# Kernel optimization log

Hardware: AMD Instinct MI355X
Metric: run time of the kernel (lower is better)

## Reference

```python
import jax, jax.numpy as jnp
import numpy as np


def setup_inputs() -> dict:
    key = jax.random.key(0)
    k1, k2 = jax.random.split(key)
    B, C, N, M = 8, 3, 4096, 4096
    source_point_cloud = jax.random.normal(k1, (B, C, N), dtype=jnp.float32)
    target_point_cloud = jax.random.normal(k2, (B, C, M), dtype=jnp.float32)
    return {"source_point_cloud": source_point_cloud,
            "target_point_cloud": target_point_cloud}


def _nn_indices(source, target):
    # source: [B,3,N], target: [B,3,M]
    # squared Euclidean distance: |s|^2 + |t|^2 - 2 s.t  (monotone in true distance,
    # so argmin matches the KD-tree nearest-neighbor query)
    s2 = jnp.sum(source * source, axis=1)               # [B,N]
    t2 = jnp.sum(target * target, axis=1)               # [B,M]
    cross = jnp.einsum('bcn,bcm->bnm', source, target)  # [B,N,M]
    d2 = s2[:, :, None] + t2[:, None, :] - 2.0 * cross  # [B,N,M]
    return jnp.argmin(d2, axis=2)                       # [B,N]


def reference(source_point_cloud, target_point_cloud):
    # Per-batch: nearest target point for each source point, then mean MSE.
    idx = _nn_indices(source_point_cloud, target_point_cloud)        # [B,N]
    # gather matched target points: [B,3,N]
    matched = jnp.take_along_axis(target_point_cloud, idx[:, None, :], axis=2)
    diff = source_point_cloud - matched
    # MSELoss over the (1,3,N) batch slice -> mean over 3*N elements; one scalar per batch
    loss_per_batch = jnp.mean(diff * diff, axis=(1, 2))              # [B]
    return loss_per_batch
```

## Files before the change

kernel.cpp:

```cpp
#include <hip/hip_runtime.h>


#define B_ 8
#define N_ 4096
#define CH 4096
#define BS 12288
#define TQ 512
#define BIG 3.4e38f

__global__ __launch_bounds__(512, 8)
void nn_loss_main(const float* __restrict__ src,
                  const float* __restrict__ tgt,
                  float* __restrict__ partial) {
    __shared__ __align__(16) char smem[8 * TQ * 4];
    float4* stage = (float4*)smem;
    float*  red   = (float*)smem;

    const int tid  = threadIdx.x;
    const int blk  = blockIdx.x;
    const int b    = blk >> 6;
    const int e    = (blk >> 3) & 7;
    const int sgrp = blk & 7;
    const int ls   = tid & 63;
    const int w    = tid >> 6;

    {
        const float* tb = tgt + b * BS;
        const int m = (e << 9) + tid;
        float x = tb[m], y = tb[m + CH], z = tb[m + 2 * CH];
        stage[tid] = make_float4(x, y, z, x * x + y * y + z * z);
    }

    const float* sb = src + b * BS;
    float ax[8], ay[8], az[8];
    #pragma unroll
    for (int j = 0; j < 8; ++j) {
        int n = (sgrp << 9) + (j << 6) + ls;
        ax[j] = -2.0f * sb[n];
        ay[j] = -2.0f * sb[n + CH];
        az[j] = -2.0f * sb[n + 2 * CH];
    }

    __syncthreads();

    float best[8];
    #pragma unroll
    for (int j = 0; j < 8; ++j) best[j] = BIG;

    const float4* tp = stage + (w << 6);
    #pragma unroll 2
    for (int i = 0; i < 64; i += 2) {
        float4 t0 = tp[i];
        float4 t1 = tp[i + 1];
        #pragma unroll
        for (int j = 0; j < 8; ++j) {
            float d0 = fmaf(ax[j], t0.x, fmaf(ay[j], t0.y, fmaf(az[j], t0.z, t0.w)));
            float d1 = fmaf(ax[j], t1.x, fmaf(ay[j], t1.y, fmaf(az[j], t1.z, t1.w)));
            best[j] = fminf(fminf(best[j], d0), d1);
        }
    }

    __syncthreads();

    #pragma unroll
    for (int j = 0; j < 8; ++j) {
        float s2 = 0.25f * fmaf(ax[j], ax[j], fmaf(ay[j], ay[j], az[j] * az[j]));
        red[(w << 9) + (j << 6) + ls] = best[j] + s2;
    }

    __syncthreads();

    float mn = red[tid];
    #pragma unroll
    for (int v = 1; v < 8; ++v)
        mn = fminf(mn, red[(v << 9) + tid]);
    partial[(e << 15) + (b << 12) + (sgrp << 9) + tid] = mn;
}

__global__ __launch_bounds__(1024)
void reduce_kernel(const float* __restrict__ partial,
                   float* __restrict__ out) {
    const int b = blockIdx.x;
    const int tid = threadIdx.x;

    float acc = 0.0f;
    #pragma unroll
    for (int j = 0; j < 4; ++j) {
        int base = (b << 12) + (j << 10) + tid;
        float mn = partial[base];
        #pragma unroll
        for (int e = 1; e < 8; ++e)
            mn = fminf(mn, partial[(e << 15) + base]);
        acc += mn;
    }

    #pragma unroll
    for (int off = 32; off > 0; off >>= 1)
        acc += __shfl_down(acc, off, 64);

    __shared__ float red[16];
    if ((tid & 63) == 0) red[tid >> 6] = acc;
    __syncthreads();
    if (tid == 0) {
        float v = 0.0f;
        #pragma unroll
        for (int k = 0; k < 16; ++k) v += red[k];
        out[b] = v * (1.0f / (3.0f * (float)N_));
    }
}

extern "C" void kernel_launch(void* const* d_in, const int* in_sizes, int n_in,
                              void* d_out, int out_size, void* d_ws, size_t ws_size,
                              hipStream_t stream) {
    const float* src = (const float*)d_in[0];
    const float* tgt = (const float*)d_in[1];
    float* out = (float*)d_out;
    float* partial = (float*)d_ws;

    nn_loss_main<<<512, 512, 0, stream>>>(src, tgt, partial);
    reduce_kernel<<<B_, 1024, 0, stream>>>(partial, out);
}
```

Before: 68.62 us.

## Fuse reduction into main kernel via cooperative grid sync and atomics

Merges the separate reduction kernel into the distance/min kernel using a cooperative launch and a grid-wide barrier. After the barrier, 64 blocks each min-reduce over the eight target-chunk partials and atomically add their scaled sum into the output. The output is zeroed inside the kernel before the barrier. This removes a second kernel launch and its gap, but adds grid-sync cost and cooperative-launch overhead, and makes the float summation order nondeterministic.

```diff
diff --git a/kernel.cpp b/kernel.cpp
--- a/kernel.cpp
+++ b/kernel.cpp
@@ -1,4 +1,7 @@
 #include <hip/hip_runtime.h>
+#include <hip/hip_cooperative_groups.h>
+
+namespace cg = cooperative_groups;
 
 
 #define B_ 8
@@ -9,9 +12,10 @@
 #define BIG 3.4e38f
 
 __global__ __launch_bounds__(512, 8)
-void nn_loss_main(const float* __restrict__ src,
-                  const float* __restrict__ tgt,
-                  float* __restrict__ partial) {
+void nn_loss_fused(const float* __restrict__ src,
+                   const float* __restrict__ tgt,
+                   float* __restrict__ partial,
+                   float* __restrict__ out) {
     __shared__ __align__(16) char smem[8 * TQ * 4];
     float4* stage = (float4*)smem;
     float*  red   = (float*)smem;
@@ -23,6 +27,8 @@
     const int sgrp = blk & 7;
     const int ls   = tid & 63;
     const int w    = tid >> 6;
+
+    if (blk == 0 && tid < B_) out[tid] = 0.0f;
 
     {
         const float* tb = tgt + b * BS;
@@ -75,37 +81,30 @@
     for (int v = 1; v < 8; ++v)
         mn = fminf(mn, red[(v << 9) + tid]);
     partial[(e << 15) + (b << 12) + (sgrp << 9) + tid] = mn;
-}
 
-__global__ __launch_bounds__(1024)
-void reduce_kernel(const float* __restrict__ partial,
-                   float* __restrict__ out) {
-    const int b = blockIdx.x;
-    const int tid = threadIdx.x;
+    cg::this_grid().sync();
 
-    float acc = 0.0f;
-    #pragma unroll
-    for (int j = 0; j < 4; ++j) {
-        int base = (b << 12) + (j << 10) + tid;
-        float mn = partial[base];
+    if (blk < 64) {
+        const int b2 = blk >> 3;
+        const int g2 = blk & 7;
+        const int base = (b2 << 12) + (g2 << 9) + tid;
+        float v0 = partial[base];
         #pragma unroll
-        for (int e = 1; e < 8; ++e)
-            mn = fminf(mn, partial[(e << 15) + base]);
-        acc += mn;
-    }
+        for (int e2 = 1; e2 < 8; ++e2)
+            v0 = fminf(v0, partial[(e2 << 15) + base]);
 
-    #pragma unroll
-    for (int off = 32; off > 0; off >>= 1)
-        acc += __shfl_down(acc, off, 64);
+        #pragma unroll
+        for (int off = 32; off > 0; off >>= 1)
+            v0 += __shfl_down(v0, off, 64);
 
-    __shared__ float red[16];
-    if ((tid & 63) == 0) red[tid >> 6] = acc;
-    __syncthreads();
-    if (tid == 0) {
-        float v = 0.0f;
-        #pragma unroll
-        for (int k = 0; k < 16; ++k) v += red[k];
-        out[b] = v * (1.0f / (3.0f * (float)N_));
+        if (ls == 0) red[w] = v0;
+        __syncthreads();
+        if (tid == 0) {
+            float s = 0.0f;
+            #pragma unroll
+            for (int k = 0; k < 8; ++k) s += red[k];
+            atomicAdd(&out[b2], s * (1.0f / (3.0f * (float)N_)));
+        }
     }
 }
 
@@ -117,6 +116,7 @@
     float* out = (float*)d_out;
     float* partial = (float*)d_ws;
 
-    nn_loss_main<<<512, 512, 0, stream>>>(src, tgt, partial);
-    reduce_kernel<<<B_, 1024, 0, stream>>>(partial, out);
+    void* args[] = {(void*)&src, (void*)&tgt, (void*)&partial, (void*)&out};
+    hipLaunchCooperativeKernel(reinterpret_cast<void*>(nn_loss_fused),
+                               dim3(512), dim3(512), args, 0, stream);
 }
```

Result: slower. 112.0 us (+63.3%).

## Split target chunks into 16 slices and parallelize final reduction with atomics

Applied to the files above, without the earlier changes.

The main kernel now launches 1024 blocks, each covering 256 target points instead of 512, which doubles grid parallelism and halves per-block compute. The reduce kernel spreads its work over 64 blocks that each reduce 16 partial minima and atomically add into the output, which is zeroed by an added memset. The cost is twice the partial-minimum traffic, an extra memset launch, and float atomics that make the summation order nondeterministic.

```diff
diff --git a/kernel.cpp b/kernel.cpp
--- a/kernel.cpp
+++ b/kernel.cpp
@@ -5,28 +5,29 @@
 #define N_ 4096
 #define CH 4096
 #define BS 12288
-#define TQ 512
+#define TQ 256
+#define NE 16
 #define BIG 3.4e38f
 
 __global__ __launch_bounds__(512, 8)
 void nn_loss_main(const float* __restrict__ src,
                   const float* __restrict__ tgt,
                   float* __restrict__ partial) {
-    __shared__ __align__(16) char smem[8 * TQ * 4];
+    __shared__ __align__(16) char smem[8 * 512 * 4];
     float4* stage = (float4*)smem;
     float*  red   = (float*)smem;
 
     const int tid  = threadIdx.x;
     const int blk  = blockIdx.x;
-    const int b    = blk >> 6;
-    const int e    = (blk >> 3) & 7;
+    const int b    = blk >> 7;
+    const int e    = (blk >> 3) & 15;
     const int sgrp = blk & 7;
     const int ls   = tid & 63;
     const int w    = tid >> 6;
 
-    {
+    if (tid < TQ) {
         const float* tb = tgt + b * BS;
-        const int m = (e << 9) + tid;
+        const int m = (e << 8) + tid;
         float x = tb[m], y = tb[m + CH], z = tb[m + 2 * CH];
         stage[tid] = make_float4(x, y, z, x * x + y * y + z * z);
     }
@@ -47,9 +48,9 @@
     #pragma unroll
     for (int j = 0; j < 8; ++j) best[j] = BIG;
 
-    const float4* tp = stage + (w << 6);
+    const float4* tp = stage + (w << 5);
     #pragma unroll 2
-    for (int i = 0; i < 64; i += 2) {
+    for (int i = 0; i < 32; i += 2) {
         float4 t0 = tp[i];
         float4 t1 = tp[i + 1];
         #pragma unroll
@@ -77,35 +78,34 @@
     partial[(e << 15) + (b << 12) + (sgrp << 9) + tid] = mn;
 }
 
-__global__ __launch_bounds__(1024)
+__global__ __launch_bounds__(512)
 void reduce_kernel(const float* __restrict__ partial,
                    float* __restrict__ out) {
-    const int b = blockIdx.x;
+    const int blk = blockIdx.x;
+    const int b   = blk >> 3;
+    const int g   = blk & 7;
     const int tid = threadIdx.x;
+    const int ls  = tid & 63;
+    const int w   = tid >> 6;
 
-    float acc = 0.0f;
+    const int base = (b << 12) + (g << 9) + tid;
+    float mn = partial[base];
     #pragma unroll
-    for (int j = 0; j < 4; ++j) {
-        int base = (b << 12) + (j << 10) + tid;
-        float mn = partial[base];
-        #pragma unroll
-        for (int e = 1; e < 8; ++e)
-            mn = fminf(mn, partial[(e << 15) + base]);
-        acc += mn;
-    }
+    for (int e = 1; e < NE; ++e)
+        mn = fminf(mn, partial[(e << 15) + base]);
 
     #pragma unroll
     for (int off = 32; off > 0; off >>= 1)
-        acc += __shfl_down(acc, off, 64);
+        mn += __shfl_down(mn, off, 64);
 
-    __shared__ float red[16];
-    if ((tid & 63) == 0) red[tid >> 6] = acc;
+    __shared__ float red[8];
+    if (ls == 0) red[w] = mn;
     __syncthreads();
     if (tid == 0) {
-        float v = 0.0f;
+        float s = 0.0f;
         #pragma unroll
-        for (int k = 0; k < 16; ++k) v += red[k];
-        out[b] = v * (1.0f / (3.0f * (float)N_));
+        for (int k = 0; k < 8; ++k) s += red[k];
+        atomicAdd(&out[b], s * (1.0f / (3.0f * (float)N_)));
     }
 }
 
@@ -117,6 +117,7 @@
     float* out = (float*)d_out;
     float* partial = (float*)d_ws;
 
-    nn_loss_main<<<512, 512, 0, stream>>>(src, tgt, partial);
-    reduce_kernel<<<B_, 1024, 0, stream>>>(partial, out);
+    hipMemsetAsync(out, 0, B_ * sizeof(float), stream);
+    nn_loss_main<<<1024, 512, 0, stream>>>(src, tgt, partial);
+    reduce_kernel<<<64, 512, 0, stream>>>(partial, out);
 }
```

Result: no change. 70.00 us (+2.0%).
